# Kernel tuning notes

Measured on AMD Instinct MI355X. Metric: run time of the kernel, lower is better.

## Reference

```python
import jax, jax.numpy as jnp
import numpy as np

NUM_FEATURES = 16
NUM_CLASSES = 4
HIDDEN = 128
NUM_LAYERS = 2
BN_EPS = 1e-5


def setup_inputs() -> dict:
    key = jax.random.key(0)
    ks = jax.random.split(key, 12)
    B, S, N, F, E = 8, 12, 5000, NUM_FEATURES, 40000
    H, L, C = HIDDEN, NUM_LAYERS, NUM_CLASSES
    x_seq = jax.random.normal(ks[0], (B, S, N, F), dtype=jnp.float32)
    edge_index = jax.random.randint(ks[1], (2, E), 0, N, dtype=jnp.int32)
    edge_weight = jax.random.uniform(ks[2], (E,), dtype=jnp.float32)
    def glorot(k, shape):
        fan_in, fan_out = shape[0], shape[-1]
        lim = jnp.sqrt(6.0 / (fan_in + fan_out)).astype(jnp.float32)
        return jax.random.uniform(k, shape, jnp.float32, -lim, lim)
    lin_in_W = glorot(ks[3], (F, H))
    lin_in_b = jnp.zeros((H,), jnp.float32)
    # per layer: 3 GCNConvs with weight [(H+H), H]
    convW = glorot(ks[4], (L, 3, 2 * H, H))
    convB = jnp.zeros((L, 3, H), jnp.float32)
    bn_gamma = jnp.ones((H,), jnp.float32)
    bn_beta = jnp.zeros((H,), jnp.float32)
    lin_out_W = glorot(ks[5], (H, C))
    lin_out_b = jnp.zeros((C,), jnp.float32)
    return {
        "x_seq": x_seq, "edge_index": edge_index, "edge_weight": edge_weight,
        "lin_in_W": lin_in_W, "lin_in_b": lin_in_b,
        "convW": convW, "convB": convB,
        "bn_gamma": bn_gamma, "bn_beta": bn_beta,
        "lin_out_W": lin_out_W, "lin_out_b": lin_out_b,
    }


def _batch_static_graph(edge_index, edge_weight, batch_size, num_nodes):
    E = edge_index.shape[1]
    shift = (jnp.arange(batch_size, dtype=edge_index.dtype) * num_nodes)  # [B]
    shift = jnp.repeat(shift, E)  # [B*E]
    bei = jnp.tile(edge_index, (1, batch_size)) + shift[None, :]
    bew = jnp.tile(edge_weight, batch_size)
    return bei, bew


def _gcn_norm(edge_index, edge_weight, num_nodes):
    # PyG GCNConv default: add self-loops (weight 1), sym normalization.
    loop = jnp.arange(num_nodes, dtype=edge_index.dtype)
    row = jnp.concatenate([edge_index[0], loop])
    col = jnp.concatenate([edge_index[1], loop])
    w = jnp.concatenate([edge_weight, jnp.ones((num_nodes,), edge_weight.dtype)])
    deg = jax.ops.segment_sum(w, col, num_segments=num_nodes)
    dis = jnp.where(deg > 0, jax.lax.rsqrt(jnp.where(deg > 0, deg, 1.0)), 0.0)
    norm = dis[row] * w * dis[col]
    return row, col, norm


def reference(x_seq, edge_index, edge_weight, lin_in_W, lin_in_b,
              convW, convB, bn_gamma, bn_beta, lin_out_W, lin_out_b):
    B, S, N, F = x_seq.shape
    H = lin_in_W.shape[1]
    L = convW.shape[0]
    bei, bew = _batch_static_graph(edge_index, edge_weight, B, N)
    total = B * N
    row, col, norm = _gcn_norm(bei, bew, total)
    # [S, total, F]
    xs = jnp.transpose(x_seq, (1, 0, 2, 3)).reshape(S, total, F)

    def gconv(x, W, b):
        xw = x @ W                                # [total, H]
        msg = norm[:, None] * xw[row]             # [E', H]
        return jax.ops.segment_sum(msg, col, num_segments=total) + b

    def step(h_all, x_t):
        x_t = jax.nn.relu(x_t @ lin_in_W + lin_in_b)
        new_h = []
        for l in range(L):
            h = h_all[l]
            combined = jnp.concatenate([x_t, h], axis=1)
            r = jax.nn.sigmoid(gconv(combined, convW[l, 0], convB[l, 0]))
            u = jax.nn.sigmoid(gconv(combined, convW[l, 1], convB[l, 1]))
            combined_r = jnp.concatenate([x_t, r * h], axis=1)
            c = jnp.tanh(gconv(combined_r, convW[l, 2], convB[l, 2]))
            h_new = u * h + (1.0 - u) * c
            new_h.append(h_new)
            x_t = h_new  # dropout is identity in eval mode
        return jnp.stack(new_h), None

    h0 = jnp.zeros((L, total, H), x_seq.dtype)
    h_all, _ = jax.lax.scan(step, h0, xs)
    h_final = h_all[-1]
    # BatchNorm over node dimension (training-mode batch statistics)
    mean = jnp.mean(h_final, axis=0)
    var = jnp.var(h_final, axis=0)
    h_final = (h_final - mean) * jax.lax.rsqrt(var + BN_EPS) * bn_gamma + bn_beta
    h_final = jax.nn.relu(h_final)
    out = h_final @ lin_out_W + lin_out_b            # [total, C]
    out = out.reshape(B, N, -1)
    return jax.nn.log_softmax(out, axis=-1)
```

## Files before the change

kernel.cpp:

```cpp
#include <hip/hip_runtime.h>
#include <cstdint>
#include <cstddef>

#define NN 5000
#define EE 40000
#define BATCH 8
#define SS 12
#define FF 16
#define HH 128
#define TOTAL 40000
#define CC 4


typedef __attribute__((ext_vector_type(8))) short short8;
typedef __attribute__((ext_vector_type(4))) float f32x4;

__device__ __forceinline__ unsigned short f2bf(float f) {
  union { float f; unsigned u; } v; v.f = f;
  unsigned r = v.u + 0x7fff + ((v.u >> 16) & 1);
  return (unsigned short)(r >> 16);
}
__device__ __forceinline__ float bf2f(unsigned short b) {
  union { unsigned u; float f; } v; v.u = ((unsigned)b) << 16;
  return v.f;
// ... 22 lines not shown
                                             const int* __restrict__ csr_src,
                                             const float* __restrict__ csr_w,
                                             const float* __restrict__ dis,
                                             int n, int bb, int fo, float* acc) {
  float sn = dis[n]; sn *= sn;
  size_t rowSelf = (size_t)(n << 3) + bb;
#pragma unroll
  for (int k = 0; k < 16; k++) acc[k] = 0.f;
  {
    float ws = sn * sc[n];
    uint4 qv = *(const uint4*)&Gq[rowSelf * 128 + fo];
    qfma16(acc, qv, ws);
  }
  int e0 = offs[n], e1 = offs[n + 1];
  int e = e0;
  for (; e + 1 < e1; e += 2) {
    int s0 = csr_src[e], s1 = csr_src[e + 1];
    float w0 = csr_w[e] * sc[s0];
    float w1 = csr_w[e + 1] * sc[s1];
    uint4 qa = *(const uint4*)&Gq[(((size_t)s0 << 3) + bb) * 128 + fo];
    uint4 qb = *(const uint4*)&Gq[(((size_t)s1 << 3) + bb) * 128 + fo];
    qfma16(acc, qa, w0);
    qfma16(acc, qb, w1);
  }
  if (e < e1) {
    int s0 = csr_src[e];
    float w0 = csr_w[e] * sc[s0];
    uint4 qa = *(const uint4*)&Gq[(((size_t)s0 << 3) + bb) * 128 + fo];
    qfma16(acc, qa, w0);
  }
}


__global__ void deg_cnt_kernel(const int* __restrict__ ei, const float* __restrict__ ew,
                               float* __restrict__ deg, int* __restrict__ cnt) {
  int e = blockIdx.x * 256 + threadIdx.x;
  if (e < EE) {
    int col = ei[EE + e];
    atomicAdd(&deg[col], ew[e]);
    atomicAdd(&cnt[col], 1);
  }
}

__global__ void dis_kernel(const float* __restrict__ deg, float* __restrict__ dis) {
  int n = blockIdx.x * 256 + threadIdx.x;
// ... 68 lines not shown
    float xv = xp[ff];
    float4 w0 = *(const float4*)&W[ff * HH + fh * 8];
    float4 w1 = *(const float4*)&W[ff * HH + fh * 8 + 4];
    a0.x += xv * w0.x; a0.y += xv * w0.y; a0.z += xv * w0.z; a0.w += xv * w0.w;
    a1.x += xv * w1.x; a1.y += xv * w1.y; a1.z += xv * w1.z; a1.w += xv * w1.w;
  }
  uint4 o;
  o.x = (unsigned)f2bf(fmaxf(a0.x, 0.f)) | ((unsigned)f2bf(fmaxf(a0.y, 0.f)) << 16);
  o.y = (unsigned)f2bf(fmaxf(a0.z, 0.f)) | ((unsigned)f2bf(fmaxf(a0.w, 0.f)) << 16);
  o.z = (unsigned)f2bf(fmaxf(a1.x, 0.f)) | ((unsigned)f2bf(fmaxf(a1.y, 0.f)) << 16);
  o.w = (unsigned)f2bf(fmaxf(a1.z, 0.f)) | ((unsigned)f2bf(fmaxf(a1.w, 0.f)) << 16);
  *(uint4*)&xt[(size_t)row * 128 + fh * 8] = o;
}


template <int NTW, int HALVES>
__device__ __forceinline__ void gemm_body(unsigned short* As, float* sInv,
                                          const unsigned short* __restrict__ Wp,
                                          signed char* __restrict__ qA,
                                          signed char* __restrict__ qB,
                                          float* __restrict__ sA,
                                          float* __restrict__ sB,
                                          int rowBase, int tid) {
  int wv = tid >> 6, lane = tid & 63;
  int m = lane & 15, q = lane >> 4;
  f32x4 acc[4][NTW];
#pragma unroll
  for (int i = 0; i < 4; i++)
#pragma unroll
    for (int j = 0; j < NTW; j++) acc[i][j] = (f32x4)(0.0f);
  const unsigned short* wbase = Wp + ((size_t)(wv * NTW) * 8 * 64 + lane) * 8;
#pragma unroll
  for (int ks = 0; ks < 8; ks++) {
    short8 a[4];
#pragma unroll
    for (int mt = 0; mt < 4; mt++)
      a[mt] = *(const short8*)&As[(mt * 16 + m) * 264 + ks * 32 + q * 8];
#pragma unroll
    for (int nt = 0; nt < NTW; nt++) {
      short8 b = *(const short8*)(wbase + (size_t)(nt * 8 + ks) * 64 * 8);
#pragma unroll
      for (int mt = 0; mt < 4; mt++)
        acc[mt][nt] = __builtin_amdgcn_mfma_f32_16x16x32_bf16(a[mt], b, acc[mt][nt], 0, 0, 0);
    }
  }
  constexpr int NC = NTW * 64;
  constexpr int CST = NC + 8;
  __syncthreads();
#pragma unroll
  for (int mt = 0; mt < 4; mt++)
#pragma unroll
    for (int nt = 0; nt < NTW; nt++) {
      int col = (wv * NTW + nt) * 16 + m;
#pragma unroll
      for (int i = 0; i < 4; i++)
        As[(mt * 16 + q * 4 + i) * CST + col] = f2bf(acc[mt][nt][i]);
    }
  __syncthreads();
  {
    constexpr int G = 8 * HALVES;
    constexpr int TPG = 256 / G;
    constexpr int CPT = 128 / TPG;
    int g = tid / TPG, j = tid % TPG;
    int node = g / HALVES;
    int half = g % HALVES;
    int c0 = half * 128 + j * CPT;
    float mx = 0.f;
#pragma unroll
    for (int r = 0; r < 8; r++) {
      const unsigned short* rp = &As[(node * 8 + r) * CST + c0];
#pragma unroll
      for (int k = 0; k < CPT; k++) mx = fmaxf(mx, fabsf(bf2f(rp[k])));
    }
#pragma unroll
    for (int off = TPG / 2; off; off >>= 1)
      mx = fmaxf(mx, __shfl_down(mx, off, TPG));
    if (j == 0) {
      sInv[g] = (mx > 0.f) ? (127.0f / mx) : 0.f;
      int gn = (rowBase >> 3) + node;
      float sc = mx * (1.0f / 127.0f);
      if (HALVES == 2) { if (half == 0) sA[gn] = sc; else sB[gn] = sc; }
      else sA[gn] = sc;
    }
  }
  __syncthreads();
  constexpr int CPQ = NC / 16;
  for (int c = tid; c < 64 * CPQ; c += 256) {
    int row = c / CPQ, cc = c % CPQ;
    int node = row >> 3;
    int half = (HALVES == 2) ? (cc >> 3) : 0;
    float inv = sInv[node * HALVES + half];
    const unsigned short* p = &As[row * CST + cc * 16];
    unsigned ow[4];
#pragma unroll
    for (int d = 0; d < 4; d++) {
      unsigned w = 0;
#pragma unroll
      for (int k = 0; k < 4; k++) {
        int qv = __float2int_rn(bf2f(p[d * 4 + k]) * inv);
        w |= ((unsigned)(qv & 255)) << (8 * k);
      }
      ow[d] = w;
    }
    signed char* dst = (half ? qB : qA) + (size_t)(rowBase + row) * 128 + (cc & 7) * 16;
    uint4 v; v.x = ow[0]; v.y = ow[1]; v.z = ow[2]; v.w = ow[3];
    *(uint4*)dst = v;
  }
}


template <int NTW, int HALVES>
__global__ __launch_bounds__(256) void gemm_mfma_q(const unsigned short* __restrict__ A1,
                                                   const unsigned short* __restrict__ A2,
                                                   const unsigned short* __restrict__ Wp,
                                                   signed char* __restrict__ qA,
                                                   signed char* __restrict__ qB,
                                                   float* __restrict__ sA,
                                                   float* __restrict__ sB) {
  __shared__ unsigned short As[64 * 264];
  __shared__ float sInv[16];
  int rowBase = blockIdx.x * 64;
  int tid = threadIdx.x;
  for (int c = tid; c < 2048; c += 256) {
    int row = c >> 5; int rest = c & 31; int half = rest >> 4; int sub = rest & 15;
    const unsigned short* src = (half ? A2 : A1) + ((size_t)(rowBase + row) * 128 + sub * 8);
    *(uint4*)&As[row * 264 + half * 128 + sub * 8] = *(const uint4*)src;
  }
  __syncthreads();
  gemm_body<NTW, HALVES>(As, sInv, Wp, qA, qB, sA, sB, rowBase, tid);
}


__global__ __launch_bounds__(256) void fused_cand_q(
    const signed char* __restrict__ GqR, const signed char* __restrict__ GqU,
    const float* __restrict__ sR, const float* __restrict__ sU,
    const int* __restrict__ offs, const int* __restrict__ csr_src,
    const float* __restrict__ csr_w, const float* __restrict__ dis,
    const float* __restrict__ bRU, const unsigned short* __restrict__ h,
    unsigned short* __restrict__ u_out,
    const unsigned short* __restrict__ A1, const unsigned short* __restrict__ Wp,
    signed char* __restrict__ Cq, float* __restrict__ sC) {
  __shared__ unsigned short As[64 * 264];
  __shared__ float sInv[16];
  int tid = threadIdx.x;
  int wv = tid >> 6, lane = tid & 63;
  int rowBase = blockIdx.x * 64, gn0 = rowBase >> 3;
  int bb = lane >> 3, fo = (lane & 7) << 4;
  for (int c = tid; c < 1024; c += 256) {
    int row = c >> 4, sub = c & 15;
    *(uint4*)&As[row * 264 + sub * 8] =
        *(const uint4*)&A1[(size_t)(rowBase + row) * 128 + sub * 8];
  }
#pragma unroll
  for (int uu = 0; uu < 4; uu++) {
    int unit = (wv << 2) + uu;
    int node8 = unit >> 1, half = unit & 1;
    int n = gn0 + node8;
    float acc[16];
    gather_accum(half ? GqU : GqR, half ? sU : sR, offs, csr_src, csr_w, dis, n, bb, fo, acc);
    const float* bias = bRU + half * 128 + fo;
    float v[16];
#pragma unroll
    for (int k = 0; k < 16; k++)
      v[k] = 1.0f / (1.0f + __expf(-(acc[k] + bias[k])));
    size_t rowSelf = ((size_t)n << 3) + bb;
    if (half == 0) {
      uint4 h0 = *(const uint4*)&h[rowSelf * 128 + fo];
      uint4 h1 = *(const uint4*)&h[rowSelf * 128 + fo + 8];
      float hv[16];
      hv[0] = bflo(h0.x); hv[1] = bfhi(h0.x); hv[2] = bflo(h0.y); hv[3] = bfhi(h0.y);
      hv[4] = bflo(h0.z); hv[5] = bfhi(h0.z); hv[6] = bflo(h0.w); hv[7] = bfhi(h0.w);
      hv[8] = bflo(h1.x); hv[9] = bfhi(h1.x); hv[10] = bflo(h1.y); hv[11] = bfhi(h1.y);
      hv[12] = bflo(h1.z); hv[13] = bfhi(h1.z); hv[14] = bflo(h1.w); hv[15] = bfhi(h1.w);
      unsigned ow[8];
#pragma unroll
      for (int d = 0; d < 8; d++)
        ow[d] = (unsigned)f2bf(v[2 * d] * hv[2 * d]) |
                ((unsigned)f2bf(v[2 * d + 1] * hv[2 * d + 1]) << 16);
      uint4 o0; o0.x = ow[0]; o0.y = ow[1]; o0.z = ow[2]; o0.w = ow[3];
      uint4 o1; o1.x = ow[4]; o1.y = ow[5]; o1.z = ow[6]; o1.w = ow[7];
      int lr = node8 * 8 + bb;
      *(uint4*)&As[lr * 264 + 128 + fo] = o0;
      *(uint4*)&As[lr * 264 + 128 + fo + 8] = o1;
    } else {
      unsigned ow[8];
#pragma unroll
      for (int d = 0; d < 8; d++)
        ow[d] = (unsigned)f2bf(v[2 * d]) | ((unsigned)f2bf(v[2 * d + 1]) << 16);
      uint4 o0; o0.x = ow[0]; o0.y = ow[1]; o0.z = ow[2]; o0.w = ow[3];
      uint4 o1; o1.x = ow[4]; o1.y = ow[5]; o1.z = ow[6]; o1.w = ow[7];
      *(uint4*)&u_out[rowSelf * 128 + fo] = o0;
      *(uint4*)&u_out[rowSelf * 128 + fo + 8] = o1;
    }
  }
  __syncthreads();
  gemm_body<2, 1>(As, sInv, Wp, Cq, Cq, sC, sC, rowBase, tid);
}


__global__ __launch_bounds__(256) void fused_gates_q(
    const signed char* __restrict__ Cq, const float* __restrict__ sC,
    const int* __restrict__ offs, const int* __restrict__ csr_src,
    const float* __restrict__ csr_w, const float* __restrict__ dis,
    const float* __restrict__ bC, const unsigned short* __restrict__ u_in,
    unsigned short* __restrict__ h_io,
    const unsigned short* __restrict__ A2src, const unsigned short* __restrict__ Wp,
    signed char* __restrict__ GqRo, signed char* __restrict__ GqUo,
    float* __restrict__ sRo, float* __restrict__ sUo) {
  __shared__ unsigned short As[64 * 264];
  __shared__ float sInv[16];
  int tid = threadIdx.x;
  int wv = tid >> 6, lane = tid & 63;
  int rowBase = blockIdx.x * 64, gn0 = rowBase >> 3;
  int bb = lane >> 3, fo = (lane & 7) << 4;
  for (int c = tid; c < 1024; c += 256) {
    int row = c >> 4, sub = c & 15;
    *(uint4*)&As[row * 264 + 128 + sub * 8] =
        *(const uint4*)&A2src[(size_t)(rowBase + row) * 128 + sub * 8];
  }
#pragma unroll
  for (int uu = 0; uu < 2; uu++) {
    int node8 = (wv << 1) + uu;
    int n = gn0 + node8;
    float acc[16];
    gather_accum(Cq, sC, offs, csr_src, csr_w, dis, n, bb, fo, acc);
    size_t rowSelf = ((size_t)n << 3) + bb;
    uint4 u0 = *(const uint4*)&u_in[rowSelf * 128 + fo];
    uint4 u1 = *(const uint4*)&u_in[rowSelf * 128 + fo + 8];
    uint4 h0 = *(const uint4*)&h_io[rowSelf * 128 + fo];
    uint4 h1 = *(const uint4*)&h_io[rowSelf * 128 + fo + 8];
    float uv[16], hv[16];
    uv[0] = bflo(u0.x); uv[1] = bfhi(u0.x); uv[2] = bflo(u0.y); uv[3] = bfhi(u0.y);
    uv[4] = bflo(u0.z); uv[5] = bfhi(u0.z); uv[6] = bflo(u0.w); uv[7] = bfhi(u0.w);
    uv[8] = bflo(u1.x); uv[9] = bfhi(u1.x); uv[10] = bflo(u1.y); uv[11] = bfhi(u1.y);
    uv[12] = bflo(u1.z); uv[13] = bfhi(u1.z); uv[14] = bflo(u1.w); uv[15] = bfhi(u1.w);
    hv[0] = bflo(h0.x); hv[1] = bfhi(h0.x); hv[2] = bflo(h0.y); hv[3] = bfhi(h0.y);
    hv[4] = bflo(h0.z); hv[5] = bfhi(h0.z); hv[6] = bflo(h0.w); hv[7] = bfhi(h0.w);
    hv[8] = bflo(h1.x); hv[9] = bfhi(h1.x); hv[10] = bflo(h1.y); hv[11] = bfhi(h1.y);
    hv[12] = bflo(h1.z); hv[13] = bfhi(h1.z); hv[14] = bflo(h1.w); hv[15] = bfhi(h1.w);
    const float* bp = bC + fo;
    float nv[16];
#pragma unroll
    for (int k = 0; k < 16; k++) {
      float val = acc[k] + bp[k];
      float c = 1.0f - 2.0f / (__expf(2.0f * val) + 1.0f);
      nv[k] = uv[k] * hv[k] + (1.0f - uv[k]) * c;
    }
    unsigned ow[8];
#pragma unroll
    for (int d = 0; d < 8; d++)
      ow[d] = (unsigned)f2bf(nv[2 * d]) | ((unsigned)f2bf(nv[2 * d + 1]) << 16);
    uint4 o0; o0.x = ow[0]; o0.y = ow[1]; o0.z = ow[2]; o0.w = ow[3];
    uint4 o1; o1.x = ow[4]; o1.y = ow[5]; o1.z = ow[6]; o1.w = ow[7];
    *(uint4*)&h_io[rowSelf * 128 + fo] = o0;
    *(uint4*)&h_io[rowSelf * 128 + fo + 8] = o1;
    int lr = node8 * 8 + bb;
    *(uint4*)&As[lr * 264 + fo] = o0;
    *(uint4*)&As[lr * 264 + fo + 8] = o1;
  }
  __syncthreads();
  gemm_body<4, 2>(As, sInv, Wp, GqRo, GqUo, sRo, sUo, rowBase, tid);
}


__global__ __launch_bounds__(256) void fused_gates_lin_q(
    const signed char* __restrict__ Cq, const float* __restrict__ sC,
    const int* __restrict__ offs, const int* __restrict__ csr_src,
    const float* __restrict__ csr_w, const float* __restrict__ dis,
    const float* __restrict__ bC, const unsigned short* __restrict__ u_in,
    unsigned short* __restrict__ h_io,
    const float* __restrict__ x_seq, const float* __restrict__ Win,
    const float* __restrict__ bin, unsigned short* __restrict__ xt_out,
    const unsigned short* __restrict__ A2src, const unsigned short* __restrict__ Wp,
    signed char* __restrict__ GqRo, signed char* __restrict__ GqUo,
    float* __restrict__ sRo, float* __restrict__ sUo, int t_next) {
  __shared__ unsigned short As[64 * 264];
  __shared__ float sInv[16];
  int tid = threadIdx.x;
  int wv = tid >> 6, lane = tid & 63;
  int rowBase = blockIdx.x * 64, gn0 = rowBase >> 3;
  int bb = lane >> 3, fo = (lane & 7) << 4;
  for (int c = tid; c < 1024; c += 256) {
    int row = c >> 4, sub = c & 15;
    *(uint4*)&As[row * 264 + 128 + sub * 8] =
        *(const uint4*)&A2src[(size_t)(rowBase + row) * 128 + sub * 8];
  }
#pragma unroll
  for (int uu = 0; uu < 2; uu++) {
    int node8 = (wv << 1) + uu;
    int n = gn0 + node8;
    float acc[16];
    gather_accum(Cq, sC, offs, csr_src, csr_w, dis, n, bb, fo, acc);
    size_t rowSelf = ((size_t)n << 3) + bb;
    uint4 u0 = *(const uint4*)&u_in[rowSelf * 128 + fo];
    uint4 u1 = *(const uint4*)&u_in[rowSelf * 128 + fo + 8];
    uint4 h0 = *(const uint4*)&h_io[rowSelf * 128 + fo];
    uint4 h1 = *(const uint4*)&h_io[rowSelf * 128 + fo + 8];
    float uv[16], hv[16];
    uv[0] = bflo(u0.x); uv[1] = bfhi(u0.x); uv[2] = bflo(u0.y); uv[3] = bfhi(u0.y);
    uv[4] = bflo(u0.z); uv[5] = bfhi(u0.z); uv[6] = bflo(u0.w); uv[7] = bfhi(u0.w);
    uv[8] = bflo(u1.x); uv[9] = bfhi(u1.x); uv[10] = bflo(u1.y); uv[11] = bfhi(u1.y);
    uv[12] = bflo(u1.z); uv[13] = bfhi(u1.z); uv[14] = bflo(u1.w); uv[15] = bfhi(u1.w);
    hv[0] = bflo(h0.x); hv[1] = bfhi(h0.x); hv[2] = bflo(h0.y); hv[3] = bfhi(h0.y);
    hv[4] = bflo(h0.z); hv[5] = bfhi(h0.z); hv[6] = bflo(h0.w); hv[7] = bfhi(h0.w);
    hv[8] = bflo(h1.x); hv[9] = bfhi(h1.x); hv[10] = bflo(h1.y); hv[11] = bfhi(h1.y);
    hv[12] = bflo(h1.z); hv[13] = bfhi(h1.z); hv[14] = bflo(h1.w); hv[15] = bfhi(h1.w);
    const float* bp = bC + fo;
    float nv[16];
#pragma unroll
    for (int k = 0; k < 16; k++) {
      float val = acc[k] + bp[k];
      float c = 1.0f - 2.0f / (__expf(2.0f * val) + 1.0f);
      nv[k] = uv[k] * hv[k] + (1.0f - uv[k]) * c;
    }
    unsigned ow[8];
#pragma unroll
    for (int d = 0; d < 8; d++)
      ow[d] = (unsigned)f2bf(nv[2 * d]) | ((unsigned)f2bf(nv[2 * d + 1]) << 16);
    uint4 o0; o0.x = ow[0]; o0.y = ow[1]; o0.z = ow[2]; o0.w = ow[3];
    uint4 o1; o1.x = ow[4]; o1.y = ow[5]; o1.z = ow[6]; o1.w = ow[7];
    *(uint4*)&h_io[rowSelf * 128 + fo] = o0;
    *(uint4*)&h_io[rowSelf * 128 + fo + 8] = o1;
  }
  for (int c = tid; c < 1024; c += 256) {
    int row = c >> 4, fh = c & 15;
    int grow = rowBase + row;
    int n2 = grow >> 3, bbv = grow & 7;
    const float* xp = x_seq + (((size_t)bbv * SS + t_next) * NN + n2) * FF;
    float4 a0 = *(const float4*)&bin[fh * 8];
    float4 a1 = *(const float4*)&bin[fh * 8 + 4];
#pragma unroll
    for (int ff = 0; ff < FF; ff++) {
      float xv = xp[ff];
      float4 w0 = *(const float4*)&Win[ff * HH + fh * 8];
      float4 w1 = *(const float4*)&Win[ff * HH + fh * 8 + 4];
      a0.x += xv * w0.x; a0.y += xv * w0.y; a0.z += xv * w0.z; a0.w += xv * w0.w;
      a1.x += xv * w1.x; a1.y += xv * w1.y; a1.z += xv * w1.z; a1.w += xv * w1.w;
    }
    uint4 o;
    o.x = (unsigned)f2bf(fmaxf(a0.x, 0.f)) | ((unsigned)f2bf(fmaxf(a0.y, 0.f)) << 16);
    o.y = (unsigned)f2bf(fmaxf(a0.z, 0.f)) | ((unsigned)f2bf(fmaxf(a0.w, 0.f)) << 16);
    o.z = (unsigned)f2bf(fmaxf(a1.x, 0.f)) | ((unsigned)f2bf(fmaxf(a1.y, 0.f)) << 16);
    o.w = (unsigned)f2bf(fmaxf(a1.z, 0.f)) | ((unsigned)f2bf(fmaxf(a1.w, 0.f)) << 16);
    *(uint4*)&As[row * 264 + fh * 8] = o;
    *(uint4*)&xt_out[(size_t)grow * 128 + fh * 8] = o;
  }
  __syncthreads();
  gemm_body<4, 2>(As, sInv, Wp, GqRo, GqUo, sRo, sUo, rowBase, tid);
}


__global__ __launch_bounds__(256) void scatter_c_update_q(
    const signed char* __restrict__ Cq, const float* __restrict__ sC,
    const int* __restrict__ offs, const int* __restrict__ csr_src,
    const float* __restrict__ csr_w, const float* __restrict__ dis,
    const float* __restrict__ bC, const unsigned short* __restrict__ u,
    unsigned short* __restrict__ h) {
  int tid = threadIdx.x;
  int wv = tid >> 6, lane = tid & 63;
  int n = blockIdx.x * 4 + wv;
  int bb = lane >> 3;
  int fo = (lane & 7) << 4;
  float acc[16];
  gather_accum(Cq, sC, offs, csr_src, csr_w, dis, n, bb, fo, acc);
  size_t rowSelf = (size_t)(n << 3) + bb;
  uint4 u0 = *(const uint4*)&u[rowSelf * 128 + fo];
  uint4 u1 = *(const uint4*)&u[rowSelf * 128 + fo + 8];
  uint4 h0 = *(const uint4*)&h[rowSelf * 128 + fo];
  uint4 h1 = *(const uint4*)&h[rowSelf * 128 + fo + 8];
  float uv[16], hv[16];
  uv[0] = bflo(u0.x); uv[1] = bfhi(u0.x); uv[2] = bflo(u0.y); uv[3] = bfhi(u0.y);
  uv[4] = bflo(u0.z); uv[5] = bfhi(u0.z); uv[6] = bflo(u0.w); uv[7] = bfhi(u0.w);
  uv[8] = bflo(u1.x); uv[9] = bfhi(u1.x); uv[10] = bflo(u1.y); uv[11] = bfhi(u1.y);
  uv[12] = bflo(u1.z); uv[13] = bfhi(u1.z); uv[14] = bflo(u1.w); uv[15] = bfhi(u1.w);
  hv[0] = bflo(h0.x); hv[1] = bfhi(h0.x); hv[2] = bflo(h0.y); hv[3] = bfhi(h0.y);
  hv[4] = bflo(h0.z); hv[5] = bfhi(h0.z); hv[6] = bflo(h0.w); hv[7] = bfhi(h0.w);
  hv[8] = bflo(h1.x); hv[9] = bfhi(h1.x); hv[10] = bflo(h1.y); hv[11] = bfhi(h1.y);
  hv[12] = bflo(h1.z); hv[13] = bfhi(h1.z); hv[14] = bflo(h1.w); hv[15] = bfhi(h1.w);
  const float* bp = bC + fo;
  float nv[16];
#pragma unroll
  for (int k = 0; k < 16; k++) {
    float val = acc[k] + bp[k];
    float c = 1.0f - 2.0f / (__expf(2.0f * val) + 1.0f);
    nv[k] = uv[k] * hv[k] + (1.0f - uv[k]) * c;
  }
  unsigned ow[8];
#pragma unroll
  for (int d = 0; d < 8; d++)
    ow[d] = (unsigned)f2bf(nv[2 * d]) | ((unsigned)f2bf(nv[2 * d + 1]) << 16);
  uint4 o0; o0.x = ow[0]; o0.y = ow[1]; o0.z = ow[2]; o0.w = ow[3];
  uint4 o1; o1.x = ow[4]; o1.y = ow[5]; o1.z = ow[6]; o1.w = ow[7];
  *(uint4*)&h[rowSelf * 128 + fo] = o0;
  *(uint4*)&h[rowSelf * 128 + fo + 8] = o1;
}


__global__ __launch_bounds__(256) void bn_stats_kernel(const unsigned short* __restrict__ h,
                                                       float* __restrict__ sums) {
  __shared__ float ls[512];
  int tid = threadIdx.x;
  float s = 0.f, sq = 0.f;
  for (size_t idx = (size_t)blockIdx.x * 256 + tid; idx < (size_t)TOTAL * HH;
       idx += (size_t)gridDim.x * 256) {
    float v = bf2f(h[idx]);
    s += v; sq += v * v;
  }
  ls[tid] = s; ls[256 + tid] = sq;
  __syncthreads();
// ... 76 lines not shown
  int*   cursor  = (int*)alloc(NN * 4);
  int*   csr_src = (int*)alloc(EE * 4);
  float* csr_w   = (float*)alloc(EE * 4);
  float* sums    = (float*)alloc(256 * 4);
  float* sR      = (float*)alloc(NN * 4);
  float* sU      = (float*)alloc(NN * 4);
  float* sC      = (float*)alloc(NN * 4);
  unsigned short* Wp = (unsigned short*)alloc(6 * 32768 * 2);
  const size_t NH = (size_t)TOTAL * HH;
  unsigned short* h0 = (unsigned short*)alloc(NH * 2);
  unsigned short* h1 = (unsigned short*)alloc(NH * 2);
  unsigned short* xt = (unsigned short*)alloc(NH * 2);
  unsigned short* ub = (unsigned short*)alloc(NH * 2);
  signed char* GqR = (signed char*)alloc(NH);
  signed char* GqU = (signed char*)alloc(NH);
  signed char* Cq  = GqR;

  hipMemsetAsync(deg, 0, NN * 4, stream);
  hipMemsetAsync(cnt, 0, NN * 4, stream);
  hipMemsetAsync(cursor, 0, NN * 4, stream);
  hipMemsetAsync(sums, 0, 256 * 4, stream);
  hipMemsetAsync(h0, 0, NH * 2, stream);
  hipMemsetAsync(h1, 0, NH * 2, stream);

  deg_cnt_kernel<<<(EE + 255) / 256, 256, 0, stream>>>(ei, ew, deg, cnt);
  dis_kernel<<<(NN + 255) / 256, 256, 0, stream>>>(deg, dis);
  scan_kernel<<<1, 256, 0, stream>>>(cnt, offs);
  fill_csr_kernel<<<(EE + 255) / 256, 256, 0, stream>>>(ei, ew, dis, offs, cursor, csr_src, csr_w);
  prepack_kernel<<<24576 / 256, 256, 0, stream>>>(convW, Wp);

  const unsigned short* Wg0 = Wp;
  const unsigned short* Wc0 = Wp + (size_t)2 * 32768;
  const unsigned short* Wg1 = Wp + (size_t)3 * 32768;
  const unsigned short* Wc1 = Wp + (size_t)5 * 32768;
  const float* bRU0 = convB;
  const float* bC0  = convB + 2 * HH;
  const float* bRU1 = convB + 3 * HH;
  const float* bC1  = convB + 5 * HH;

  lin_in_kernel<<<TOTAL * 16 / 256, 256, 0, stream>>>(x_seq, Win, bin, xt, 0);
  gemm_mfma_q<4, 2><<<TOTAL / 64, 256, 0, stream>>>(xt, h0, Wg0, GqR, GqU, sR, sU);

  for (int t = 0; t < SS; t++) {
    fused_cand_q<<<TOTAL / 64, 256, 0, stream>>>(GqR, GqU, sR, sU, offs, csr_src, csr_w,
                                                 dis, bRU0, h0, ub, xt, Wc0, Cq, sC);
    fused_gates_q<<<TOTAL / 64, 256, 0, stream>>>(Cq, sC, offs, csr_src, csr_w, dis,
                                                  bC0, ub, h0, h1, Wg1, GqR, GqU, sR, sU);
    fused_cand_q<<<TOTAL / 64, 256, 0, stream>>>(GqR, GqU, sR, sU, offs, csr_src, csr_w,
                                                 dis, bRU1, h1, ub, h0, Wc1, Cq, sC);
    if (t < SS - 1) {
      fused_gates_lin_q<<<TOTAL / 64, 256, 0, stream>>>(Cq, sC, offs, csr_src, csr_w, dis,
                                                        bC1, ub, h1, x_seq, Win, bin, xt,
                                                        h0, Wg0, GqR, GqU, sR, sU, t + 1);
    } else {
      scatter_c_update_q<<<NN / 4, 256, 0, stream>>>(Cq, sC, offs, csr_src, csr_w,
                                                     dis, bC1, ub, h1);
    }
  }

  bn_stats_kernel<<<256, 256, 0, stream>>>(h1, sums);
  final_kernel<<<TOTAL / 4, 256, 0, stream>>>(h1, sums, gamma, beta, Wout, bout, out);
}
```

Baseline: 1.824 ms.

## Halve row tile to 32 with 512-thread blocks and specialize waves per task

The fused GCN-GRU kernels now process 32 rows per block with 512 threads instead of 64 rows with 256. Each wave handles one gather unit, and in the gates kernels half the waves gather while the other half stage the A2 tile or compute lin_in, so these run concurrently. The per-node quantization max now uses one wave per group with a full-wave shuffle, and the edge gather loop is unrolled by 4 for more loads in flight. Cq gets its own buffer instead of aliasing GqR, which costs extra memory. The smaller tiles mean fewer MFMA rows per wave and twice as many blocks, which raises scheduling overhead.

```diff
diff --git a/kernel.cpp b/kernel.cpp
--- a/kernel.cpp
+++ b/kernel.cpp
@@ -60,21 +60,63 @@
   }
   int e0 = offs[n], e1 = offs[n + 1];
   int e = e0;
-  for (; e + 1 < e1; e += 2) {
+  for (; e + 3 < e1; e += 4) {
     int s0 = csr_src[e], s1 = csr_src[e + 1];
+    int s2 = csr_src[e + 2], s3 = csr_src[e + 3];
     float w0 = csr_w[e] * sc[s0];
     float w1 = csr_w[e + 1] * sc[s1];
+    float w2 = csr_w[e + 2] * sc[s2];
+    float w3 = csr_w[e + 3] * sc[s3];
     uint4 qa = *(const uint4*)&Gq[(((size_t)s0 << 3) + bb) * 128 + fo];
     uint4 qb = *(const uint4*)&Gq[(((size_t)s1 << 3) + bb) * 128 + fo];
+    uint4 qc = *(const uint4*)&Gq[(((size_t)s2 << 3) + bb) * 128 + fo];
+    uint4 qd = *(const uint4*)&Gq[(((size_t)s3 << 3) + bb) * 128 + fo];
     qfma16(acc, qa, w0);
     qfma16(acc, qb, w1);
-  }
-  if (e < e1) {
+    qfma16(acc, qc, w2);
+    qfma16(acc, qd, w3);
+  }
+  for (; e < e1; e++) {
     int s0 = csr_src[e];
     float w0 = csr_w[e] * sc[s0];
     uint4 qa = *(const uint4*)&Gq[(((size_t)s0 << 3) + bb) * 128 + fo];
     qfma16(acc, qa, w0);
   }
+}
+
+__device__ __forceinline__ void gru_combine_store(const float* acc, const float* bp,
+                                                  const unsigned short* __restrict__ u_in,
+                                                  unsigned short* __restrict__ h_io,
+                                                  size_t rowSelf, int fo,
+                                                  uint4& o0, uint4& o1) {
+  uint4 u0 = *(const uint4*)&u_in[rowSelf * 128 + fo];
+  uint4 u1 = *(const uint4*)&u_in[rowSelf * 128 + fo + 8];
+  uint4 h0 = *(const uint4*)&h_io[rowSelf * 128 + fo];
+  uint4 h1 = *(const uint4*)&h_io[rowSelf * 128 + fo + 8];
+  float uv[16], hv[16];
+  uv[0] = bflo(u0.x); uv[1] = bfhi(u0.x); uv[2] = bflo(u0.y); uv[3] = bfhi(u0.y);
+  uv[4] = bflo(u0.z); uv[5] = bfhi(u0.z); uv[6] = bflo(u0.w); uv[7] = bfhi(u0.w);
+  uv[8] = bflo(u1.x); uv[9] = bfhi(u1.x); uv[10] = bflo(u1.y); uv[11] = bfhi(u1.y);
+  uv[12] = bflo(u1.z); uv[13] = bfhi(u1.z); uv[14] = bflo(u1.w); uv[15] = bfhi(u1.w);
+  hv[0] = bflo(h0.x); hv[1] = bfhi(h0.x); hv[2] = bflo(h0.y); hv[3] = bfhi(h0.y);
+  hv[4] = bflo(h0.z); hv[5] = bfhi(h0.z); hv[6] = bflo(h0.w); hv[7] = bfhi(h0.w);
+  hv[8] = bflo(h1.x); hv[9] = bfhi(h1.x); hv[10] = bflo(h1.y); hv[11] = bfhi(h1.y);
+  hv[12] = bflo(h1.z); hv[13] = bfhi(h1.z); hv[14] = bflo(h1.w); hv[15] = bfhi(h1.w);
+  float nv[16];
+#pragma unroll
+  for (int k = 0; k < 16; k++) {
+    float val = acc[k] + bp[k];
+    float c = 1.0f - 2.0f / (__expf(2.0f * val) + 1.0f);
+    nv[k] = uv[k] * hv[k] + (1.0f - uv[k]) * c;
+  }
+  unsigned ow[8];
+#pragma unroll
+  for (int d = 0; d < 8; d++)
+    ow[d] = (unsigned)f2bf(nv[2 * d]) | ((unsigned)f2bf(nv[2 * d + 1]) << 16);
+  o0.x = ow[0]; o0.y = ow[1]; o0.z = ow[2]; o0.w = ow[3];
+  o1.x = ow[4]; o1.y = ow[5]; o1.z = ow[6]; o1.w = ow[7];
+  *(uint4*)&h_io[rowSelf * 128 + fo] = o0;
+  *(uint4*)&h_io[rowSelf * 128 + fo + 8] = o1;
 }
 
 
@@ -173,7 +215,7 @@
 }
 
 
-template <int NTW, int HALVES>
+template <int MT, int NTW, int HALVES, int NTHREADS>
 __device__ __forceinline__ void gemm_body(unsigned short* As, float* sInv,
                                           const unsigned short* __restrict__ Wp,
                                           signed char* __restrict__ qA,
@@ -181,33 +223,35 @@
                                           float* __restrict__ sA,
                                           float* __restrict__ sB,
                                           int rowBase, int tid) {
+  constexpr int NWAVES = NTHREADS / 64;
+  constexpr int NC = NTW * 16 * NWAVES;
+  constexpr int R = MT * 16;
   int wv = tid >> 6, lane = tid & 63;
   int m = lane & 15, q = lane >> 4;
-  f32x4 acc[4][NTW];
-#pragma unroll
-  for (int i = 0; i < 4; i++)
+  f32x4 acc[MT][NTW];
+#pragma unroll
+  for (int i = 0; i < MT; i++)
 #pragma unroll
     for (int j = 0; j < NTW; j++) acc[i][j] = (f32x4)(0.0f);
   const unsigned short* wbase = Wp + ((size_t)(wv * NTW) * 8 * 64 + lane) * 8;
 #pragma unroll
   for (int ks = 0; ks < 8; ks++) {
-    short8 a[4];
-#pragma unroll
-    for (int mt = 0; mt < 4; mt++)
+    short8 a[MT];
+#pragma unroll
+    for (int mt = 0; mt < MT; mt++)
       a[mt] = *(const short8*)&As[(mt * 16 + m) * 264 + ks * 32 + q * 8];
 #pragma unroll
     for (int nt = 0; nt < NTW; nt++) {
       short8 b = *(const short8*)(wbase + (size_t)(nt * 8 + ks) * 64 * 8);
 #pragma unroll
-      for (int mt = 0; mt < 4; mt++)
+      for (int mt = 0; mt < MT; mt++)
         acc[mt][nt] = __builtin_amdgcn_mfma_f32_16x16x32_bf16(a[mt], b, acc[mt][nt], 0, 0, 0);
     }
   }
-  constexpr int NC = NTW * 64;
   constexpr int CST = NC + 8;
   __syncthreads();
 #pragma unroll
-  for (int mt = 0; mt < 4; mt++)
+  for (int mt = 0; mt < MT; mt++)
 #pragma unroll
     for (int nt = 0; nt < NTW; nt++) {
       int col = (wv * NTW + nt) * 16 + m;
@@ -216,35 +260,30 @@
         As[(mt * 16 + q * 4 + i) * CST + col] = f2bf(acc[mt][nt][i]);
     }
   __syncthreads();
-  {
-    constexpr int G = 8 * HALVES;
-    constexpr int TPG = 256 / G;
-    constexpr int CPT = 128 / TPG;
-    int g = tid / TPG, j = tid % TPG;
-    int node = g / HALVES;
-    int half = g % HALVES;
-    int c0 = half * 128 + j * CPT;
+  constexpr int G = (R / 8) * HALVES;
+  static_assert(G <= NWAVES, "one wave per quant group");
+  if (wv < G) {
+    int node = wv / HALVES, half = wv % HALVES;
+    int c0 = half * 128 + lane * 2;
     float mx = 0.f;
 #pragma unroll
     for (int r = 0; r < 8; r++) {
       const unsigned short* rp = &As[(node * 8 + r) * CST + c0];
-#pragma unroll
-      for (int k = 0; k < CPT; k++) mx = fmaxf(mx, fabsf(bf2f(rp[k])));
-    }
-#pragma unroll
-    for (int off = TPG / 2; off; off >>= 1)
-      mx = fmaxf(mx, __shfl_down(mx, off, TPG));
-    if (j == 0) {
-      sInv[g] = (mx > 0.f) ? (127.0f / mx) : 0.f;
+      mx = fmaxf(mx, fmaxf(fabsf(bf2f(rp[0])), fabsf(bf2f(rp[1]))));
+    }
+#pragma unroll
+    for (int off = 32; off; off >>= 1) mx = fmaxf(mx, __shfl_down(mx, off));
+    if (lane == 0) {
+      sInv[wv] = (mx > 0.f) ? (127.0f / mx) : 0.f;
       int gn = (rowBase >> 3) + node;
-      float sc = mx * (1.0f / 127.0f);
-      if (HALVES == 2) { if (half == 0) sA[gn] = sc; else sB[gn] = sc; }
-      else sA[gn] = sc;
+      float scv = mx * (1.0f / 127.0f);
+      if (HALVES == 2) { if (half == 0) sA[gn] = scv; else sB[gn] = scv; }
+      else sA[gn] = scv;
     }
   }
   __syncthreads();
   constexpr int CPQ = NC / 16;
-  for (int c = tid; c < 64 * CPQ; c += 256) {
+  for (int c = tid; c < R * CPQ; c += NTHREADS) {
     int row = c / CPQ, cc = c % CPQ;
     int node = row >> 3;
     int half = (HALVES == 2) ? (cc >> 3) : 0;
@@ -269,28 +308,28 @@
 
 
 template <int NTW, int HALVES>
-__global__ __launch_bounds__(256) void gemm_mfma_q(const unsigned short* __restrict__ A1,
+__global__ __launch_bounds__(512) void gemm_mfma_q(const unsigned short* __restrict__ A1,
                                                    const unsigned short* __restrict__ A2,
                                                    const unsigned short* __restrict__ Wp,
                                                    signed char* __restrict__ qA,
                                                    signed char* __restrict__ qB,
                                                    float* __restrict__ sA,
                                                    float* __restrict__ sB) {
-  __shared__ unsigned short As[64 * 264];
-  __shared__ float sInv[16];
-  int rowBase = blockIdx.x * 64;
+  __shared__ unsigned short As[32 * 264];
+  __shared__ float sInv[8];
+  int rowBase = blockIdx.x * 32;
   int tid = threadIdx.x;
-  for (int c = tid; c < 2048; c += 256) {
+  for (int c = tid; c < 1024; c += 512) {
     int row = c >> 5; int rest = c & 31; int half = rest >> 4; int sub = rest & 15;
     const unsigned short* src = (half ? A2 : A1) + ((size_t)(rowBase + row) * 128 + sub * 8);
     *(uint4*)&As[row * 264 + half * 128 + sub * 8] = *(const uint4*)src;
   }
   __syncthreads();
-  gemm_body<NTW, HALVES>(As, sInv, Wp, qA, qB, sA, sB, rowBase, tid);
-}
-
-
-__global__ __launch_bounds__(256) void fused_cand_q(
+  gemm_body<2, NTW, HALVES, 512>(As, sInv, Wp, qA, qB, sA, sB, rowBase, tid);
+}
+
+
+__global__ __launch_bounds__(512) void fused_cand_q(
     const signed char* __restrict__ GqR, const signed char* __restrict__ GqU,
     const float* __restrict__ sR, const float* __restrict__ sU,
     const int* __restrict__ offs, const int* __restrict__ csr_src,
@@ -299,65 +338,61 @@
     unsigned short* __restrict__ u_out,
     const unsigned short* __restrict__ A1, const unsigned short* __restrict__ Wp,
     signed char* __restrict__ Cq, float* __restrict__ sC) {
-  __shared__ unsigned short As[64 * 264];
-  __shared__ float sInv[16];
+  __shared__ unsigned short As[32 * 264];
+  __shared__ float sInv[8];
   int tid = threadIdx.x;
   int wv = tid >> 6, lane = tid & 63;
-  int rowBase = blockIdx.x * 64, gn0 = rowBase >> 3;
+  int rowBase = blockIdx.x * 32, gn0 = rowBase >> 3;
   int bb = lane >> 3, fo = (lane & 7) << 4;
-  for (int c = tid; c < 1024; c += 256) {
-    int row = c >> 4, sub = c & 15;
+  {
+    int row = tid >> 4, sub = tid & 15;
     *(uint4*)&As[row * 264 + sub * 8] =
         *(const uint4*)&A1[(size_t)(rowBase + row) * 128 + sub * 8];
   }
-#pragma unroll
-  for (int uu = 0; uu < 4; uu++) {
-    int unit = (wv << 2) + uu;
-    int node8 = unit >> 1, half = unit & 1;
-    int n = gn0 + node8;
-    float acc[16];
-    gather_accum(half ? GqU : GqR, half ? sU : sR, offs, csr_src, csr_w, dis, n, bb, fo, acc);
-    const float* bias = bRU + half * 128 + fo;
-    float v[16];
-#pragma unroll
-    for (int k = 0; k < 16; k++)
-      v[k] = 1.0f / (1.0f + __expf(-(acc[k] + bias[k])));
-    size_t rowSelf = ((size_t)n << 3) + bb;
-    if (half == 0) {
-      uint4 h0 = *(const uint4*)&h[rowSelf * 128 + fo];
-      uint4 h1 = *(const uint4*)&h[rowSelf * 128 + fo + 8];
-      float hv[16];
-      hv[0] = bflo(h0.x); hv[1] = bfhi(h0.x); hv[2] = bflo(h0.y); hv[3] = bfhi(h0.y);
-      hv[4] = bflo(h0.z); hv[5] = bfhi(h0.z); hv[6] = bflo(h0.w); hv[7] = bfhi(h0.w);
-      hv[8] = bflo(h1.x); hv[9] = bfhi(h1.x); hv[10] = bflo(h1.y); hv[11] = bfhi(h1.y);
-      hv[12] = bflo(h1.z); hv[13] = bfhi(h1.z); hv[14] = bflo(h1.w); hv[15] = bfhi(h1.w);
-      unsigned ow[8];
-#pragma unroll
-      for (int d = 0; d < 8; d++)
-        ow[d] = (unsigned)f2bf(v[2 * d] * hv[2 * d]) |
-                ((unsigned)f2bf(v[2 * d + 1] * hv[2 * d + 1]) << 16);
-      uint4 o0; o0.x = ow[0]; o0.y = ow[1]; o0.z = ow[2]; o0.w = ow[3];
-      uint4 o1; o1.x = ow[4]; o1.y = ow[5]; o1.z = ow[6]; o1.w = ow[7];
-      int lr = node8 * 8 + bb;
-      *(uint4*)&As[lr * 264 + 128 + fo] = o0;
-      *(uint4*)&As[lr * 264 + 128 + fo + 8] = o1;
-    } else {
-      unsigned ow[8];
-#pragma unroll
-      for (int d = 0; d < 8; d++)
-        ow[d] = (unsigned)f2bf(v[2 * d]) | ((unsigned)f2bf(v[2 * d + 1]) << 16);
-      uint4 o0; o0.x = ow[0]; o0.y = ow[1]; o0.z = ow[2]; o0.w = ow[3];
-      uint4 o1; o1.x = ow[4]; o1.y = ow[5]; o1.z = ow[6]; o1.w = ow[7];
-      *(uint4*)&u_out[rowSelf * 128 + fo] = o0;
-      *(uint4*)&u_out[rowSelf * 128 + fo + 8] = o1;
-    }
-  }
-  __syncthreads();
-  gemm_body<2, 1>(As, sInv, Wp, Cq, Cq, sC, sC, rowBase, tid);
-}
-
-
-__global__ __launch_bounds__(256) void fused_gates_q(
+  int node8 = wv >> 1, half = wv & 1;
+  int n = gn0 + node8;
+  float acc[16];
+  gather_accum(half ? GqU : GqR, half ? sU : sR, offs, csr_src, csr_w, dis, n, bb, fo, acc);
+  const float* bias = bRU + half * 128 + fo;
+  float v[16];
+#pragma unroll
+  for (int k = 0; k < 16; k++)
+    v[k] = 1.0f / (1.0f + __expf(-(acc[k] + bias[k])));
+  size_t rowSelf = ((size_t)n << 3) + bb;
+  if (half == 0) {
+    uint4 h0 = *(const uint4*)&h[rowSelf * 128 + fo];
+    uint4 h1 = *(const uint4*)&h[rowSelf * 128 + fo + 8];
+    float hv[16];
+    hv[0] = bflo(h0.x); hv[1] = bfhi(h0.x); hv[2] = bflo(h0.y); hv[3] = bfhi(h0.y);
+    hv[4] = bflo(h0.z); hv[5] = bfhi(h0.z); hv[6] = bflo(h0.w); hv[7] = bfhi(h0.w);
+    hv[8] = bflo(h1.x); hv[9] = bfhi(h1.x); hv[10] = bflo(h1.y); hv[11] = bfhi(h1.y);
+    hv[12] = bflo(h1.z); hv[13] = bfhi(h1.z); hv[14] = bflo(h1.w); hv[15] = bfhi(h1.w);
+    unsigned ow[8];
+#pragma unroll
+    for (int d = 0; d < 8; d++)
+      ow[d] = (unsigned)f2bf(v[2 * d] * hv[2 * d]) |
+              ((unsigned)f2bf(v[2 * d + 1] * hv[2 * d + 1]) << 16);
+    uint4 o0; o0.x = ow[0]; o0.y = ow[1]; o0.z = ow[2]; o0.w = ow[3];
+    uint4 o1; o1.x = ow[4]; o1.y = ow[5]; o1.z = ow[6]; o1.w = ow[7];
+    int lr = node8 * 8 + bb;
+    *(uint4*)&As[lr * 264 + 128 + fo] = o0;
+    *(uint4*)&As[lr * 264 + 128 + fo + 8] = o1;
+  } else {
+    unsigned ow[8];
+#pragma unroll
+    for (int d = 0; d < 8; d++)
+      ow[d] = (unsigned)f2bf(v[2 * d]) | ((unsigned)f2bf(v[2 * d + 1]) << 16);
+    uint4 o0; o0.x = ow[0]; o0.y = ow[1]; o0.z = ow[2]; o0.w = ow[3];
+    uint4 o1; o1.x = ow[4]; o1.y = ow[5]; o1.z = ow[6]; o1.w = ow[7];
+    *(uint4*)&u_out[rowSelf * 128 + fo] = o0;
+    *(uint4*)&u_out[rowSelf * 128 + fo + 8] = o1;
+  }
+  __syncthreads();
+  gemm_body<2, 1, 1, 512>(As, sInv, Wp, Cq, Cq, sC, sC, rowBase, tid);
+}
+
+
+__global__ __launch_bounds__(512) void fused_gates_q(
     const signed char* __restrict__ Cq, const float* __restrict__ sC,
     const int* __restrict__ offs, const int* __restrict__ csr_src,
     const float* __restrict__ csr_w, const float* __restrict__ dis,
@@ -366,63 +401,37 @@
     const unsigned short* __restrict__ A2src, const unsigned short* __restrict__ Wp,
     signed char* __restrict__ GqRo, signed char* __restrict__ GqUo,
     float* __restrict__ sRo, float* __restrict__ sUo) {
-  __shared__ unsigned short As[64 * 264];
-  __shared__ float sInv[16];
+  __shared__ unsigned short As[32 * 264];
+  __shared__ float sInv[8];
   int tid = threadIdx.x;
   int wv = tid >> 6, lane = tid & 63;
-  int rowBase = blockIdx.x * 64, gn0 = rowBase >> 3;
+  int rowBase = blockIdx.x * 32, gn0 = rowBase >> 3;
   int bb = lane >> 3, fo = (lane & 7) << 4;
-  for (int c = tid; c < 1024; c += 256) {
-    int row = c >> 4, sub = c & 15;
-    *(uint4*)&As[row * 264 + 128 + sub * 8] =
-        *(const uint4*)&A2src[(size_t)(rowBase + row) * 128 + sub * 8];
-  }
-#pragma unroll
-  for (int uu = 0; uu < 2; uu++) {
-    int node8 = (wv << 1) + uu;
+  if (wv >= 4) {
+    int t2 = tid - 256;
+    for (int c = t2; c < 512; c += 256) {
+      int row = c >> 4, sub = c & 15;
+      *(uint4*)&As[row * 264 + 128 + sub * 8] =
+          *(const uint4*)&A2src[(size_t)(rowBase + row) * 128 + sub * 8];
+    }
+  } else {
+    int node8 = wv;
     int n = gn0 + node8;
     float acc[16];
     gather_accum(Cq, sC, offs, csr_src, csr_w, dis, n, bb, fo, acc);
     size_t rowSelf = ((size_t)n << 3) + bb;
-    uint4 u0 = *(const uint4*)&u_in[rowSelf * 128 + fo];
-    uint4 u1 = *(const uint4*)&u_in[rowSelf * 128 + fo + 8];
-    uint4 h0 = *(const uint4*)&h_io[rowSelf * 128 + fo];
-    uint4 h1 = *(const uint4*)&h_io[rowSelf * 128 + fo + 8];
-    float uv[16], hv[16];
-    uv[0] = bflo(u0.x); uv[1] = bfhi(u0.x); uv[2] = bflo(u0.y); uv[3] = bfhi(u0.y);
-    uv[4] = bflo(u0.z); uv[5] = bfhi(u0.z); uv[6] = bflo(u0.w); uv[7] = bfhi(u0.w);
-    uv[8] = bflo(u1.x); uv[9] = bfhi(u1.x); uv[10] = bflo(u1.y); uv[11] = bfhi(u1.y);
-    uv[12] = bflo(u1.z); uv[13] = bfhi(u1.z); uv[14] = bflo(u1.w); uv[15] = bfhi(u1.w);
-    hv[0] = bflo(h0.x); hv[1] = bfhi(h0.x); hv[2] = bflo(h0.y); hv[3] = bfhi(h0.y);
-    hv[4] = bflo(h0.z); hv[5] = bfhi(h0.z); hv[6] = bflo(h0.w); hv[7] = bfhi(h0.w);
-    hv[8] = bflo(h1.x); hv[9] = bfhi(h1.x); hv[10] = bflo(h1.y); hv[11] = bfhi(h1.y);
-    hv[12] = bflo(h1.z); hv[13] = bfhi(h1.z); hv[14] = bflo(h1.w); hv[15] = bfhi(h1.w);
-    const float* bp = bC + fo;
-    float nv[16];
-#pragma unroll
-    for (int k = 0; k < 16; k++) {
-      float val = acc[k] + bp[k];
-      float c = 1.0f - 2.0f / (__expf(2.0f * val) + 1.0f);
-      nv[k] = uv[k] * hv[k] + (1.0f - uv[k]) * c;
-    }
-    unsigned ow[8];
-#pragma unroll
-    for (int d = 0; d < 8; d++)
-      ow[d] = (unsigned)f2bf(nv[2 * d]) | ((unsigned)f2bf(nv[2 * d + 1]) << 16);
-    uint4 o0; o0.x = ow[0]; o0.y = ow[1]; o0.z = ow[2]; o0.w = ow[3];
-    uint4 o1; o1.x = ow[4]; o1.y = ow[5]; o1.z = ow[6]; o1.w = ow[7];
-    *(uint4*)&h_io[rowSelf * 128 + fo] = o0;
-    *(uint4*)&h_io[rowSelf * 128 + fo + 8] = o1;
+    uint4 o0, o1;
+    gru_combine_store(acc, bC + fo, u_in, h_io, rowSelf, fo, o0, o1);
     int lr = node8 * 8 + bb;
     *(uint4*)&As[lr * 264 + fo] = o0;
     *(uint4*)&As[lr * 264 + fo + 8] = o1;
   }
   __syncthreads();
-  gemm_body<4, 2>(As, sInv, Wp, GqRo, GqUo, sRo, sUo, rowBase, tid);
-}
-
-
-__global__ __launch_bounds__(256) void fused_gates_lin_q(
+  gemm_body<2, 2, 2, 512>(As, sInv, Wp, GqRo, GqUo, sRo, sUo, rowBase, tid);
+}
+
+
+__global__ __launch_bounds__(512) void fused_gates_lin_q(
     const signed char* __restrict__ Cq, const float* __restrict__ sC,
     const int* __restrict__ offs, const int* __restrict__ csr_src,
     const float* __restrict__ csr_w, const float* __restrict__ dis,
@@ -433,79 +442,53 @@
     const unsigned short* __restrict__ A2src, const unsigned short* __restrict__ Wp,
     signed char* __restrict__ GqRo, signed char* __restrict__ GqUo,
     float* __restrict__ sRo, float* __restrict__ sUo, int t_next) {
-  __shared__ unsigned short As[64 * 264];
-  __shared__ float sInv[16];
+  __shared__ unsigned short As[32 * 264];
+  __shared__ float sInv[8];
   int tid = threadIdx.x;
   int wv = tid >> 6, lane = tid & 63;
-  int rowBase = blockIdx.x * 64, gn0 = rowBase >> 3;
+  int rowBase = blockIdx.x * 32, gn0 = rowBase >> 3;
   int bb = lane >> 3, fo = (lane & 7) << 4;
-  for (int c = tid; c < 1024; c += 256) {
-    int row = c >> 4, sub = c & 15;
-    *(uint4*)&As[row * 264 + 128 + sub * 8] =
-        *(const uint4*)&A2src[(size_t)(rowBase + row) * 128 + sub * 8];
-  }
-#pragma unroll
-  for (int uu = 0; uu < 2; uu++) {
-    int node8 = (wv << 1) + uu;
+  if (wv < 4) {
+    int node8 = wv;
     int n = gn0 + node8;
     float acc[16];
     gather_accum(Cq, sC, offs, csr_src, csr_w, dis, n, bb, fo, acc);
     size_t rowSelf = ((size_t)n << 3) + bb;
-    uint4 u0 = *(const uint4*)&u_in[rowSelf * 128 + fo];
-    uint4 u1 = *(const uint4*)&u_in[rowSelf * 128 + fo + 8];
-    uint4 h0 = *(const uint4*)&h_io[rowSelf * 128 + fo];
-    uint4 h1 = *(const uint4*)&h_io[rowSelf * 128 + fo + 8];
-    float uv[16], hv[16];
-    uv[0] = bflo(u0.x); uv[1] = bfhi(u0.x); uv[2] = bflo(u0.y); uv[3] = bfhi(u0.y);
-    uv[4] = bflo(u0.z); uv[5] = bfhi(u0.z); uv[6] = bflo(u0.w); uv[7] = bfhi(u0.w);
-    uv[8] = bflo(u1.x); uv[9] = bfhi(u1.x); uv[10] = bflo(u1.y); uv[11] = bfhi(u1.y);
-    uv[12] = bflo(u1.z); uv[13] = bfhi(u1.z); uv[14] = bflo(u1.w); uv[15] = bfhi(u1.w);
-    hv[0] = bflo(h0.x); hv[1] = bfhi(h0.x); hv[2] = bflo(h0.y); hv[3] = bfhi(h0.y);
-    hv[4] = bflo(h0.z); hv[5] = bfhi(h0.z); hv[6] = bflo(h0.w); hv[7] = bfhi(h0.w);
-    hv[8] = bflo(h1.x); hv[9] = bfhi(h1.x); hv[10] = bflo(h1.y); hv[11] = bfhi(h1.y);
-    hv[12] = bflo(h1.z); hv[13] = bfhi(h1.z); hv[14] = bflo(h1.w); hv[15] = bfhi(h1.w);
-    const float* bp = bC + fo;
-    float nv[16];
-#pragma unroll
-    for (int k = 0; k < 16; k++) {
-      float val = acc[k] + bp[k];
-      float c = 1.0f - 2.0f / (__expf(2.0f * val) + 1.0f);
-      nv[k] = uv[k] * hv[k] + (1.0f - uv[k]) * c;
-    }
-    unsigned ow[8];
-#pragma unroll
-    for (int d = 0; d < 8; d++)
-      ow[d] = (unsigned)f2bf(nv[2 * d]) | ((unsigned)f2bf(nv[2 * d + 1]) << 16);
-    uint4 o0; o0.x = ow[0]; o0.y = ow[1]; o0.z = ow[2]; o0.w = ow[3];
-    uint4 o1; o1.x = ow[4]; o1.y = ow[5]; o1.z = ow[6]; o1.w = ow[7];
-    *(uint4*)&h_io[rowSelf * 128 + fo] = o0;
-    *(uint4*)&h_io[rowSelf * 128 + fo + 8] = o1;
-  }
-  for (int c = tid; c < 1024; c += 256) {
-    int row = c >> 4, fh = c & 15;
-    int grow = rowBase + row;
-    int n2 = grow >> 3, bbv = grow & 7;
-    const float* xp = x_seq + (((size_t)bbv * SS + t_next) * NN + n2) * FF;
-    float4 a0 = *(const float4*)&bin[fh * 8];
-    float4 a1 = *(const float4*)&bin[fh * 8 + 4];
-#pragma unroll
-    for (int ff = 0; ff < FF; ff++) {
-      float xv = xp[ff];
-      float4 w0 = *(const float4*)&Win[ff * HH + fh * 8];
-      float4 w1 = *(const float4*)&Win[ff * HH + fh * 8 + 4];
-      a0.x += xv * w0.x; a0.y += xv * w0.y; a0.z += xv * w0.z; a0.w += xv * w0.w;
-      a1.x += xv * w1.x; a1.y += xv * w1.y; a1.z += xv * w1.z; a1.w += xv * w1.w;
-    }
-    uint4 o;
-    o.x = (unsigned)f2bf(fmaxf(a0.x, 0.f)) | ((unsigned)f2bf(fmaxf(a0.y, 0.f)) << 16);
-    o.y = (unsigned)f2bf(fmaxf(a0.z, 0.f)) | ((unsigned)f2bf(fmaxf(a0.w, 0.f)) << 16);
-    o.z = (unsigned)f2bf(fmaxf(a1.x, 0.f)) | ((unsigned)f2bf(fmaxf(a1.y, 0.f)) << 16);
-    o.w = (unsigned)f2bf(fmaxf(a1.z, 0.f)) | ((unsigned)f2bf(fmaxf(a1.w, 0.f)) << 16);
-    *(uint4*)&As[row * 264 + fh * 8] = o;
-    *(uint4*)&xt_out[(size_t)grow * 128 + fh * 8] = o;
-  }
-  __syncthreads();
-  gemm_body<4, 2>(As, sInv, Wp, GqRo, GqUo, sRo, sUo, rowBase, tid);
+    uint4 o0, o1;
+    gru_combine_store(acc, bC + fo, u_in, h_io, rowSelf, fo, o0, o1);
+  } else {
+    int t2 = tid - 256;
+    for (int c = t2; c < 512; c += 256) {
+      int row = c >> 4, sub = c & 15;
+      *(uint4*)&As[row * 264 + 128 + sub * 8] =
+          *(const uint4*)&A2src[(size_t)(rowBase + row) * 128 + sub * 8];
+    }
+    for (int c = t2; c < 512; c += 256) {
+      int row = c >> 4, fh = c & 15;
+      int grow = rowBase + row;
+      int n2 = grow >> 3, bbv = grow & 7;
+      const float* xp = x_seq + (((size_t)bbv * SS + t_next) * NN + n2) * FF;
+      float4 a0 = *(const float4*)&bin[fh * 8];
+      float4 a1 = *(const float4*)&bin[fh * 8 + 4];
+#pragma unroll
+      for (int ff = 0; ff < FF; ff++) {
+        float xv = xp[ff];
+        float4 w0 = *(const float4*)&Win[ff * HH + fh * 8];
+        float4 w1 = *(const float4*)&Win[ff * HH + fh * 8 + 4];
+        a0.x += xv * w0.x; a0.y += xv * w0.y; a0.z += xv * w0.z; a0.w += xv * w0.w;
+        a1.x += xv * w1.x; a1.y += xv * w1.y; a1.z += xv * w1.z; a1.w += xv * w1.w;
+      }
+      uint4 o;
+      o.x = (unsigned)f2bf(fmaxf(a0.x, 0.f)) | ((unsigned)f2bf(fmaxf(a0.y, 0.f)) << 16);
+      o.y = (unsigned)f2bf(fmaxf(a0.z, 0.f)) | ((unsigned)f2bf(fmaxf(a0.w, 0.f)) << 16);
+      o.z = (unsigned)f2bf(fmaxf(a1.x, 0.f)) | ((unsigned)f2bf(fmaxf(a1.y, 0.f)) << 16);
+      o.w = (unsigned)f2bf(fmaxf(a1.z, 0.f)) | ((unsigned)f2bf(fmaxf(a1.w, 0.f)) << 16);
+      *(uint4*)&As[row * 264 + fh * 8] = o;
+      *(uint4*)&xt_out[(size_t)grow * 128 + fh * 8] = o;
+    }
+  }
+  __syncthreads();
+  gemm_body<2, 2, 2, 512>(As, sInv, Wp, GqRo, GqUo, sRo, sUo, rowBase, tid);
 }
 
 
@@ -523,35 +506,8 @@
   float acc[16];
   gather_accum(Cq, sC, offs, csr_src, csr_w, dis, n, bb, fo, acc);
   size_t rowSelf = (size_t)(n << 3) + bb;
-  uint4 u0 = *(const uint4*)&u[rowSelf * 128 + fo];
-  uint4 u1 = *(const uint4*)&u[rowSelf * 128 + fo + 8];
-  uint4 h0 = *(const uint4*)&h[rowSelf * 128 + fo];
-  uint4 h1 = *(const uint4*)&h[rowSelf * 128 + fo + 8];
-  float uv[16], hv[16];
-  uv[0] = bflo(u0.x); uv[1] = bfhi(u0.x); uv[2] = bflo(u0.y); uv[3] = bfhi(u0.y);
-  uv[4] = bflo(u0.z); uv[5] = bfhi(u0.z); uv[6] = bflo(u0.w); uv[7] = bfhi(u0.w);
-  uv[8] = bflo(u1.x); uv[9] = bfhi(u1.x); uv[10] = bflo(u1.y); uv[11] = bfhi(u1.y);
-  uv[12] = bflo(u1.z); uv[13] = bfhi(u1.z); uv[14] = bflo(u1.w); uv[15] = bfhi(u1.w);
-  hv[0] = bflo(h0.x); hv[1] = bfhi(h0.x); hv[2] = bflo(h0.y); hv[3] = bfhi(h0.y);
-  hv[4] = bflo(h0.z); hv[5] = bfhi(h0.z); hv[6] = bflo(h0.w); hv[7] = bfhi(h0.w);
-  hv[8] = bflo(h1.x); hv[9] = bfhi(h1.x); hv[10] = bflo(h1.y); hv[11] = bfhi(h1.y);
-  hv[12] = bflo(h1.z); hv[13] = bfhi(h1.z); hv[14] = bflo(h1.w); hv[15] = bfhi(h1.w);
-  const float* bp = bC + fo;
-  float nv[16];
-#pragma unroll
-  for (int k = 0; k < 16; k++) {
-    float val = acc[k] + bp[k];
-    float c = 1.0f - 2.0f / (__expf(2.0f * val) + 1.0f);
-    nv[k] = uv[k] * hv[k] + (1.0f - uv[k]) * c;
-  }
-  unsigned ow[8];
-#pragma unroll
-  for (int d = 0; d < 8; d++)
-    ow[d] = (unsigned)f2bf(nv[2 * d]) | ((unsigned)f2bf(nv[2 * d + 1]) << 16);
-  uint4 o0; o0.x = ow[0]; o0.y = ow[1]; o0.z = ow[2]; o0.w = ow[3];
-  uint4 o1; o1.x = ow[4]; o1.y = ow[5]; o1.z = ow[6]; o1.w = ow[7];
-  *(uint4*)&h[rowSelf * 128 + fo] = o0;
-  *(uint4*)&h[rowSelf * 128 + fo + 8] = o1;
+  uint4 o0, o1;
+  gru_combine_store(acc, bC + fo, u, h, rowSelf, fo, o0, o1);
 }
 
 
@@ -658,7 +614,7 @@
   unsigned short* ub = (unsigned short*)alloc(NH * 2);
   signed char* GqR = (signed char*)alloc(NH);
   signed char* GqU = (signed char*)alloc(NH);
-  signed char* Cq  = GqR;
+  signed char* Cq  = (signed char*)alloc(NH);
 
   hipMemsetAsync(deg, 0, NN * 4, stream);
   hipMemsetAsync(cnt, 0, NN * 4, stream);
@@ -683,17 +639,17 @@
   const float* bC1  = convB + 5 * HH;
 
   lin_in_kernel<<<TOTAL * 16 / 256, 256, 0, stream>>>(x_seq, Win, bin, xt, 0);
-  gemm_mfma_q<4, 2><<<TOTAL / 64, 256, 0, stream>>>(xt, h0, Wg0, GqR, GqU, sR, sU);
+  gemm_mfma_q<2, 2><<<TOTAL / 32, 512, 0, stream>>>(xt, h0, Wg0, GqR, GqU, sR, sU);
 
   for (int t = 0; t < SS; t++) {
-    fused_cand_q<<<TOTAL / 64, 256, 0, stream>>>(GqR, GqU, sR, sU, offs, csr_src, csr_w,
+    fused_cand_q<<<TOTAL / 32, 512, 0, stream>>>(GqR, GqU, sR, sU, offs, csr_src, csr_w,
                                                  dis, bRU0, h0, ub, xt, Wc0, Cq, sC);
-    fused_gates_q<<<TOTAL / 64, 256, 0, stream>>>(Cq, sC, offs, csr_src, csr_w, dis,
+    fused_gates_q<<<TOTAL / 32, 512, 0, stream>>>(Cq, sC, offs, csr_src, csr_w, dis,
                                                   bC0, ub, h0, h1, Wg1, GqR, GqU, sR, sU);
-    fused_cand_q<<<TOTAL / 64, 256, 0, stream>>>(GqR, GqU, sR, sU, offs, csr_src, csr_w,
+    fused_cand_q<<<TOTAL / 32, 512, 0, stream>>>(GqR, GqU, sR, sU, offs, csr_src, csr_w,
                                                  dis, bRU1, h1, ub, h0, Wc1, Cq, sC);
     if (t < SS - 1) {
-      fused_gates_lin_q<<<TOTAL / 64, 256, 0, stream>>>(Cq, sC, offs, csr_src, csr_w, dis,
+      fused_gates_lin_q<<<TOTAL / 32, 512, 0, stream>>>(Cq, sC, offs, csr_src, csr_w, dis,
                                                         bC1, ub, h1, x_seq, Win, bin, xt,
                                                         h0, Wg0, GqR, GqU, sR, sU, t + 1);
     } else {
```

New measurement: 1.615 ms. -11.4%, faster.
